# Kernel tuning notes

Hardware: AMD Instinct MI355X
Metric: run time of the kernel (lower is better)

Reference implementation:

```python
import jax, jax.numpy as jnp
import numpy as np

NUM_TOKENS = 14
DIM = 128
B, N = 8, 128
NUM_ROUNDS = 5


def setup_inputs() -> dict:
    key = jax.random.key(0)
    ks = jax.random.split(key, 10)
    s = 1.0 / np.sqrt(DIM)
    return {
        "tok": jax.random.randint(ks[0], (B, N), 0, NUM_TOKENS),
        "A": jax.random.uniform(ks[1], (B, N, N), dtype=jnp.float32),
        "embed": jax.random.normal(ks[2], (NUM_TOKENS, DIM), dtype=jnp.float32),
        "W1": jax.random.normal(ks[3], (DIM, 2 * DIM), dtype=jnp.float32) * s,
        "b1": jax.random.normal(ks[4], (DIM,), dtype=jnp.float32) * s,
        "W2": jax.random.normal(ks[5], (DIM, DIM), dtype=jnp.float32) * s,
        "b2": jax.random.normal(ks[6], (DIM,), dtype=jnp.float32) * s,
        "Wo1": jax.random.normal(ks[7], (DIM, DIM), dtype=jnp.float32) * s,
        "bo1": jax.random.normal(ks[8], (DIM,), dtype=jnp.float32) * s,
        "Wo2": jax.random.normal(ks[9], (10, DIM), dtype=jnp.float32) * s,
    }


def reference(tok, A, embed, W1, b1, W2, b2, Wo1, bo1, Wo2):
    # Dropout is identity (eval mode / inference reference).
    x = embed[tok]  # [B, N, D]
    d = x.shape[-1]
    # fc1 on concat(x_i, x_j) decomposes into two per-node projections:
    # fc1([x_i, x_j]) = x_i @ W1a^T + x_j @ W1b^T + b1
    W1a, W1b = W1[:, :d], W1[:, d:]
    A_t = jnp.swapaxes(A, 1, 2)  # A.transpose(1, 2)
    for _ in range(NUM_ROUNDS):
        hi = jnp.einsum("bnd,ed->bne", x, W1a)
        hj = jnp.einsum("bnd,ed->bne", x, W1b)
        # pairwise edge MLP: [B, N, N, D]
        h = jax.nn.relu(hi[:, :, None, :] + hj[:, None, :, :] + b1)
        m = jax.nn.relu(jnp.einsum("bijd,ed->bije", h, W2) + b2)
        # mask by transposed adjacency and sum over neighbors j (axis 2)
        msg = jnp.einsum("bij,bije->bie", A_t, m)
        x = x + msg
    def head(z):
        return jax.nn.relu(z @ Wo1.T + bo1) @ Wo2.T
    out = head(x[:, 0, :])                       # [B, 10]
    x_all = head(x.reshape(-1, d)).reshape(x.shape[0], x.shape[1], 10)
    return (out, x_all)
```

## Files before the change

### kernel.cpp

```cpp
#include <hip/hip_runtime.h>
#include <hip/hip_bf16.h>

#define BB 8
#define NN 128
#define DD 128

typedef __attribute__((ext_vector_type(8))) short bf16x8;
typedef __attribute__((ext_vector_type(4))) float floatx4;

__device__ __forceinline__ unsigned short f2bf(float f) {
    unsigned int bits = __float_as_uint(f);
    unsigned int r = bits + 0x7FFFu + ((bits >> 16) & 1u);
    return (unsigned short)(r >> 16);
}

#define WS_X0F   0
#define WS_X1F   131072
#define WS_W1T   262144
#define WS_W2B   279552

__global__ __launch_bounds__(256) void k_init(const int* __restrict__ tok,
                                              const float* __restrict__ embf,
                                              const float* __restrict__ W1f,
                                              const float* __restrict__ W2f,
                                              float* __restrict__ ws) {
    float* x0f = ws + WS_X0F;
    unsigned short* gw1t = (unsigned short*)(ws + WS_W1T);
    unsigned short* gw2b = (unsigned short*)(ws + WS_W2B);
    int blk = blockIdx.x, t = threadIdx.x;
    if (blk < 32) {
        int base = blk * 4096;
#pragma unroll
        for (int it = 0; it < 16; ++it) {
            int idx = base + it * 256 + t;
            int r = idx >> 7, d = idx & 127;
            x0f[idx] = embf[tok[r] * DD + d];
        }
    } else if (blk < 41) {
        int base = (blk - 32) * 4096;
#pragma unroll
        for (int it = 0; it < 16; ++it) {
            int idx = base + it * 256 + t;
            if (idx < 256 * 136) {
                int e = idx / 136, d = idx - e * 136;
                gw1t[idx] = (d < 128) ? f2bf(W1f[(e & 127) * 256 + (e >> 7) * 128 + d])
                                      : (unsigned short)0;
            }
        }
    } else {
        int base = (blk - 41) * 4096;
#pragma unroll
        for (int it = 0; it < 16; ++it) {
            int idx = base + it * 256 + t;
            if (idx < 128 * 136) {
                int e = idx / 136, d = idx - e * 136;
                gw2b[idx] = (d < 128) ? f2bf(W2f[e * 128 + d]) : (unsigned short)0;
            }
        }
    }
}

__global__ __launch_bounds__(512, 2) void k_round(const float* __restrict__ Af,
                                                  const float* __restrict__ b1f,
                                                  const float* __restrict__ b2f,
                                                  const float* __restrict__ curf,
                                                  float* __restrict__ nxtf,
                                                  const unsigned short* __restrict__ gw1t,
                                                  const unsigned short* __restrict__ gw2b) {
    __shared__ __align__(16) unsigned short w1t[256 * 136];
    __shared__ __align__(16) unsigned short w2b[128 * 136];
    __shared__ __align__(16) unsigned short xb[128 * 136];
    __shared__ __align__(16) float red[4][4][128];
    __shared__ float a_s[4][128];
    __shared__ __align__(16) float hja_s[4][128];
    __shared__ float b1s[128], b2s[128];

    int blk = blockIdx.x;
    int b = blk >> 5, g = blk & 31, i0 = g * 4;
    int t = threadIdx.x;
    int wave = t >> 6, lane = t & 63;
    int col = lane & 15, quad = lane >> 4;

    {
        const uint4* s1 = (const uint4*)gw1t; uint4* d1 = (uint4*)w1t;
#pragma unroll
        for (int it = 0; it < 9; ++it) { int idx = it * 512 + t; if (idx < 4352) d1[idx] = s1[idx]; }
        const uint4* s2 = (const uint4*)gw2b; uint4* d2 = (uint4*)w2b;
#pragma unroll
        for (int it = 0; it < 5; ++it) { int idx = it * 512 + t; if (idx < 2176) d2[idx] = s2[idx]; }
    }
    if (t < 128) { b1s[t] = b1f[t]; b2s[t] = b2f[t]; }
    a_s[t >> 7][t & 127] = Af[(b * NN + (t & 127)) * NN + i0 + (t >> 7)];

    float xown = curf[(b * NN + i0 + (t >> 7)) * DD + (t & 127)];

    const int myw = i0 >> 4;
    const int qr  = g & 3;

    const float* curb = curf + b * NN * DD;
#pragma unroll
    for (int it = 0; it < 16; ++it) {
        int idx = it * 1024 + t * 2;
        int j = idx >> 7, d = idx & 127;
        float2 v = *reinterpret_cast<const float2*>(curb + j * DD + d);
        unsigned int packed = (unsigned int)f2bf(v.x) | ((unsigned int)f2bf(v.y) << 16);
        *reinterpret_cast<unsigned int*>(&xb[j * 136 + d]) = packed;
    }
    __syncthreads();

    bf16x8 af[4];
#pragma unroll
    for (int ks = 0; ks < 4; ++ks)
        af[ks] = *reinterpret_cast<const bf16x8*>(&xb[(wave * 16 + col) * 136 + ks * 32 + quad * 8]);
    floatx4 acc1[16];
#pragma unroll
    for (int nt = 0; nt < 16; ++nt) acc1[nt] = (floatx4){0.f, 0.f, 0.f, 0.f};
#pragma unroll
    for (int nt = 0; nt < 16; ++nt)
#pragma unroll
        for (int ks = 0; ks < 4; ++ks) {
            bf16x8 bfc = *reinterpret_cast<const bf16x8*>(&w1t[(nt * 16 + col) * 136 + ks * 32 + quad * 8]);
            acc1[nt] = __builtin_amdgcn_mfma_f32_16x16x32_bf16(af[ks], bfc, acc1[nt], 0, 0, 0);
        }
    if (wave == myw && quad == qr) {
#pragma unroll
        for (int nt = 0; nt < 8; ++nt) {
            int d = nt * 16 + col;
#pragma unroll
            for (int rr = 0; rr < 4; ++rr) hja_s[rr][d] = acc1[nt][rr];
        }
    }
#pragma unroll
    for (int nt = 8; nt < 16; ++nt) {
        int d = (nt - 8) * 16 + col;
#pragma unroll
        for (int rr = 0; rr < 4; ++rr) {
            int j = wave * 16 + quad * 4 + rr;
            xb[j * 136 + d] = f2bf(acc1[nt][rr] + b1s[d]);
        }
    }
    __syncthreads();

    int we = wave & 1, wj = wave >> 1;
    int ebase = we * 64, jbase = wj * 32;
    bf16x8 bw[4][4];
#pragma unroll
    for (int et = 0; et < 4; ++et)
#pragma unroll
        for (int ks = 0; ks < 4; ++ks)
            bw[et][ks] = *reinterpret_cast<const bf16x8*>(&w2b[(ebase + et * 16 + col) * 136 + ks * 32 + quad * 8]);
#pragma unroll
    for (int ii = 0; ii < 4; ++ii) {
        floatx4 acc2[2][4];
#pragma unroll
        for (int jt = 0; jt < 2; ++jt)
#pragma unroll
            for (int et = 0; et < 4; ++et) acc2[jt][et] = (floatx4){0.f, 0.f, 0.f, 0.f};
#pragma unroll
        for (int jt = 0; jt < 2; ++jt)
#pragma unroll
            for (int ks = 0; ks < 4; ++ks) {
                int k0 = ks * 32 + quad * 8;
                union { bf16x8 v; unsigned int u[4]; } Rw, Ho;
                Rw.v = *reinterpret_cast<const bf16x8*>(&xb[(jbase + jt * 16 + col) * 136 + k0]);
                const float* hb = &hja_s[ii][k0];
#pragma unroll
                for (int p = 0; p < 4; ++p) {
                    float f0 = __uint_as_float(Rw.u[p] << 16);
                    float f1 = __uint_as_float(Rw.u[p] & 0xFFFF0000u);
                    f0 = fmaxf(f0 + hb[2 * p], 0.f);
                    f1 = fmaxf(f1 + hb[2 * p + 1], 0.f);
                    Ho.u[p] = (unsigned int)f2bf(f0) | ((unsigned int)f2bf(f1) << 16);
                }
#pragma unroll
                for (int et = 0; et < 4; ++et)
                    acc2[jt][et] = __builtin_amdgcn_mfma_f32_16x16x32_bf16(Ho.v, bw[et][ks], acc2[jt][et], 0, 0, 0);
            }
#pragma unroll
        for (int et = 0; et < 4; ++et) {
            int e = ebase + et * 16 + col;
            float be = b2s[e];
            float s = 0.f;
#pragma unroll
            for (int jt = 0; jt < 2; ++jt) {
                int j0 = jbase + jt * 16 + quad * 4;
#pragma unroll
                for (int rr = 0; rr < 4; ++rr)
                    s += a_s[ii][j0 + rr] * fmaxf(acc2[jt][et][rr] + be, 0.f);
            }
            s += __shfl_xor(s, 16, 64);
            s += __shfl_xor(s, 32, 64);
            if (quad == 0) red[wj][ii][e] = s;
        }
    }
    __syncthreads();

    {
        int ii = t >> 7, e = t & 127;
        xown += red[0][ii][e] + red[1][ii][e] + red[2][ii][e] + red[3][ii][e];
        nxtf[(b * NN + i0 + ii) * DD + e] = xown;
    }
}

__global__ __launch_bounds__(128) void k_head(const float* __restrict__ x,
                                              const float* __restrict__ Wo1f,
                                              const float* __restrict__ bo1f,
                                              const float* __restrict__ Wo2f,
                                              float* __restrict__ out) {
    __shared__ __align__(16) float zs[DD];
    __shared__ float rs[DD];
    int r = blockIdx.x;
    int t = threadIdx.x;
    zs[t] = x[r * DD + t];
    __syncthreads();
    const float4* wrow = reinterpret_cast<const float4*>(Wo1f + t * DD);
    float acc = 0.f;
#pragma unroll
    for (int d4 = 0; d4 < 32; ++d4) {
        float4 w = wrow[d4];
        acc += zs[d4 * 4 + 0] * w.x + zs[d4 * 4 + 1] * w.y
             + zs[d4 * 4 + 2] * w.z + zs[d4 * 4 + 3] * w.w;
    }
    rs[t] = fmaxf(acc + bo1f[t], 0.f);
    __syncthreads();
    if (t < 10) {
        const float* w2r = Wo2f + t * DD;
        float s = 0.f;
#pragma unroll
        for (int e2 = 0; e2 < DD; ++e2) s += rs[e2] * w2r[e2];
        int bb = r >> 7, nn = r & 127;
        out[80 + r * 10 + t] = s;
        if (nn == 0) out[bb * 10 + t] = s;
    }
}

extern "C" void kernel_launch(void* const* d_in, const int* in_sizes, int n_in,
                              void* d_out, int out_size, void* d_ws, size_t ws_size,
                              hipStream_t stream) {
    const int*   tok  = (const int*)d_in[0];
    const float* Af   = (const float*)d_in[1];
    const float* embf = (const float*)d_in[2];
    const float* W1f  = (const float*)d_in[3];
    const float* b1f  = (const float*)d_in[4];
    const float* W2f  = (const float*)d_in[5];
    const float* b2f  = (const float*)d_in[6];
    const float* Wo1f = (const float*)d_in[7];
    const float* bo1f = (const float*)d_in[8];
    const float* Wo2f = (const float*)d_in[9];

    float* ws  = (float*)d_ws;
    float* out = (float*)d_out;
    float* x0f = ws + WS_X0F;
    float* x1f = ws + WS_X1F;
    const unsigned short* gw1t = (const unsigned short*)(ws + WS_W1T);
    const unsigned short* gw2b = (const unsigned short*)(ws + WS_W2B);

    k_init<<<46, 256, 0, stream>>>(tok, embf, W1f, W2f, ws);
    for (int r = 0; r < 5; ++r) {
        const float* cf = (r & 1) ? x1f : x0f;
        float*       nf = (r & 1) ? x0f : x1f;
        k_round<<<256, 512, 0, stream>>>(Af, b1f, b2f, cf, nf, gw1t, gw2b);
    }
    k_head<<<BB * NN, 128, 0, stream>>>(x1f, Wo1f, bo1f, Wo2f, out);
}
```

Measured before the change: 169.2 us.

## Halve rows per block, drop W1 shared staging, skip redundant hi projection

Each round block now handles 2 target nodes instead of 4, doubling the grid to 512 blocks. W1 is no longer copied into shared memory; its fragments are read directly from global memory. Only the wave owning the target rows computes the hi half of the first projection. Launch bounds are raised to 4 blocks per CU. Together these cut shared memory use so more blocks can fit per CU. In exchange, each block recomputes the full hj projection and the bf16 conversion of x for only half as much edge work, and W1 reads now go to global or cache instead of LDS.

```diff
diff --git a/kernel.cpp b/kernel.cpp
--- a/kernel.cpp
+++ b/kernel.cpp
@@ -60,42 +60,39 @@
     }
 }
 
-__global__ __launch_bounds__(512, 2) void k_round(const float* __restrict__ Af,
+__global__ __launch_bounds__(512, 4) void k_round(const float* __restrict__ Af,
                                                   const float* __restrict__ b1f,
                                                   const float* __restrict__ b2f,
                                                   const float* __restrict__ curf,
                                                   float* __restrict__ nxtf,
                                                   const unsigned short* __restrict__ gw1t,
                                                   const unsigned short* __restrict__ gw2b) {
-    __shared__ __align__(16) unsigned short w1t[256 * 136];
     __shared__ __align__(16) unsigned short w2b[128 * 136];
     __shared__ __align__(16) unsigned short xb[128 * 136];
-    __shared__ __align__(16) float red[4][4][128];
-    __shared__ float a_s[4][128];
-    __shared__ __align__(16) float hja_s[4][128];
+    __shared__ __align__(16) float red[4][2][128];
+    __shared__ float a_s[2][128];
+    __shared__ __align__(16) float hja_s[2][128];
     __shared__ float b1s[128], b2s[128];
 
     int blk = blockIdx.x;
-    int b = blk >> 5, g = blk & 31, i0 = g * 4;
+    int b = blk >> 6, g = blk & 63, i0 = g * 2;
     int t = threadIdx.x;
     int wave = t >> 6, lane = t & 63;
     int col = lane & 15, quad = lane >> 4;
 
     {
-        const uint4* s1 = (const uint4*)gw1t; uint4* d1 = (uint4*)w1t;
-#pragma unroll
-        for (int it = 0; it < 9; ++it) { int idx = it * 512 + t; if (idx < 4352) d1[idx] = s1[idx]; }
         const uint4* s2 = (const uint4*)gw2b; uint4* d2 = (uint4*)w2b;
 #pragma unroll
         for (int it = 0; it < 5; ++it) { int idx = it * 512 + t; if (idx < 2176) d2[idx] = s2[idx]; }
     }
     if (t < 128) { b1s[t] = b1f[t]; b2s[t] = b2f[t]; }
-    a_s[t >> 7][t & 127] = Af[(b * NN + (t & 127)) * NN + i0 + (t >> 7)];
-
-    float xown = curf[(b * NN + i0 + (t >> 7)) * DD + (t & 127)];
+    if (t < 256) a_s[t >> 7][t & 127] = Af[(b * NN + (t & 127)) * NN + i0 + (t >> 7)];
+
+    float xown = (t < 256) ? curf[(b * NN + i0 + (t >> 7)) * DD + (t & 127)] : 0.f;
 
     const int myw = i0 >> 4;
-    const int qr  = g & 3;
+    const int qr  = (i0 >> 2) & 3;
+    const int rr0 = i0 & 3;
 
     const float* curb = curf + b * NN * DD;
 #pragma unroll
@@ -112,31 +109,45 @@
 #pragma unroll
     for (int ks = 0; ks < 4; ++ks)
         af[ks] = *reinterpret_cast<const bf16x8*>(&xb[(wave * 16 + col) * 136 + ks * 32 + quad * 8]);
-    floatx4 acc1[16];
-#pragma unroll
-    for (int nt = 0; nt < 16; ++nt) acc1[nt] = (floatx4){0.f, 0.f, 0.f, 0.f};
-#pragma unroll
-    for (int nt = 0; nt < 16; ++nt)
-#pragma unroll
-        for (int ks = 0; ks < 4; ++ks) {
-            bf16x8 bfc = *reinterpret_cast<const bf16x8*>(&w1t[(nt * 16 + col) * 136 + ks * 32 + quad * 8]);
-            acc1[nt] = __builtin_amdgcn_mfma_f32_16x16x32_bf16(af[ks], bfc, acc1[nt], 0, 0, 0);
-        }
-    if (wave == myw && quad == qr) {
+    if (wave == myw) {
+        floatx4 acca[8];
+#pragma unroll
+        for (int nt = 0; nt < 8; ++nt) acca[nt] = (floatx4){0.f, 0.f, 0.f, 0.f};
+#pragma unroll
+        for (int nt = 0; nt < 8; ++nt)
+#pragma unroll
+            for (int ks = 0; ks < 4; ++ks) {
+                bf16x8 bfc = *reinterpret_cast<const bf16x8*>(&gw1t[(nt * 16 + col) * 136 + ks * 32 + quad * 8]);
+                acca[nt] = __builtin_amdgcn_mfma_f32_16x16x32_bf16(af[ks], bfc, acca[nt], 0, 0, 0);
+            }
+        if (quad == qr) {
+#pragma unroll
+            for (int nt = 0; nt < 8; ++nt) {
+                int d = nt * 16 + col;
+                hja_s[0][d] = acca[nt][rr0];
+                hja_s[1][d] = acca[nt][rr0 + 1];
+            }
+        }
+    }
+    {
+        floatx4 accb[8];
+#pragma unroll
+        for (int nt = 0; nt < 8; ++nt) accb[nt] = (floatx4){0.f, 0.f, 0.f, 0.f};
+#pragma unroll
+        for (int nt = 0; nt < 8; ++nt)
+#pragma unroll
+            for (int ks = 0; ks < 4; ++ks) {
+                bf16x8 bfc = *reinterpret_cast<const bf16x8*>(&gw1t[((nt + 8) * 16 + col) * 136 + ks * 32 + quad * 8]);
+                accb[nt] = __builtin_amdgcn_mfma_f32_16x16x32_bf16(af[ks], bfc, accb[nt], 0, 0, 0);
+            }
 #pragma unroll
         for (int nt = 0; nt < 8; ++nt) {
             int d = nt * 16 + col;
 #pragma unroll
-            for (int rr = 0; rr < 4; ++rr) hja_s[rr][d] = acc1[nt][rr];
-        }
-    }
-#pragma unroll
-    for (int nt = 8; nt < 16; ++nt) {
-        int d = (nt - 8) * 16 + col;
-#pragma unroll
-        for (int rr = 0; rr < 4; ++rr) {
-            int j = wave * 16 + quad * 4 + rr;
-            xb[j * 136 + d] = f2bf(acc1[nt][rr] + b1s[d]);
+            for (int rr = 0; rr < 4; ++rr) {
+                int j = wave * 16 + quad * 4 + rr;
+                xb[j * 136 + d] = f2bf(accb[nt][rr] + b1s[d]);
+            }
         }
     }
     __syncthreads();
@@ -150,7 +161,7 @@
         for (int ks = 0; ks < 4; ++ks)
             bw[et][ks] = *reinterpret_cast<const bf16x8*>(&w2b[(ebase + et * 16 + col) * 136 + ks * 32 + quad * 8]);
 #pragma unroll
-    for (int ii = 0; ii < 4; ++ii) {
+    for (int ii = 0; ii < 2; ++ii) {
         floatx4 acc2[2][4];
 #pragma unroll
         for (int jt = 0; jt < 2; ++jt)
@@ -195,7 +206,7 @@
     }
     __syncthreads();
 
-    {
+    if (t < 256) {
         int ii = t >> 7, e = t & 127;
         xown += red[0][ii][e] + red[1][ii][e] + red[2][ii][e] + red[3][ii][e];
         nxtf[(b * NN + i0 + ii) * DD + e] = xown;
@@ -259,7 +270,7 @@
     for (int r = 0; r < 5; ++r) {
         const float* cf = (r & 1) ? x1f : x0f;
         float*       nf = (r & 1) ? x0f : x1f;
-        k_round<<<256, 512, 0, stream>>>(Af, b1f, b2f, cf, nf, gw1t, gw2b);
+        k_round<<<512, 512, 0, stream>>>(Af, b1f, b2f, cf, nf, gw1t, gw2b);
     }
     k_head<<<BB * NN, 128, 0, stream>>>(x1f, Wo1f, bo1f, Wo2f, out);
 }
```

Result: slower. 273.8 us (+61.9%).
